# Kernel optimization log

Hardware: AMD Instinct MI355X
Metric: run time of the kernel (lower is better)

The kernel has to match this reference:

```python
import jax, jax.numpy as jnp
import numpy as np

EPS = 1e-5

def _conv1x1(x, w):
    # x: (B, Cin, N, K), w: (Cout, Cin) -> (B, Cout, N, K)
    return jnp.einsum('oc,bcnk->bonk', w, x)

def _bn2d(x, gamma, beta):
    # eval-mode BN with running_mean=0, running_var=1 (fresh init)
    scale = gamma / jnp.sqrt(1.0 + EPS)
    return x * scale[None, :, None, None] + beta[None, :, None, None]

def setup_inputs() -> dict:
    key = jax.random.key(0)
    ks = jax.random.split(key, 10)
    B, Cin, N, K = 8, 64, 1024, 32
    Cout, M = 64, 8
    Cin2 = 2 * Cin  # kernel_input='w_neighbor'
    features = jax.random.normal(ks[0], (B, Cin, N, K), dtype=jnp.float32)
    points_xyz = jax.random.normal(ks[1], (B, 3, N, K), dtype=jnp.float32)
    # ScoreNet convs: mlp_channels [7,16,16,16,M]; first 3 have BN (no bias), last has bias
    w1 = jax.random.normal(ks[2], (16, 7), dtype=jnp.float32) * (2.0 / 7) ** 0.5
    w2 = jax.random.normal(ks[3], (16, 16), dtype=jnp.float32) * (2.0 / 16) ** 0.5
    w3 = jax.random.normal(ks[4], (16, 16), dtype=jnp.float32) * (2.0 / 16) ** 0.5
    w4 = jax.random.normal(ks[5], (M, 16), dtype=jnp.float32) * (2.0 / 16) ** 0.5
    b4 = jnp.zeros((M,), dtype=jnp.float32)
    g1 = jnp.ones((16,), jnp.float32); be1 = jnp.zeros((16,), jnp.float32)
    g2 = jnp.ones((16,), jnp.float32); be2 = jnp.zeros((16,), jnp.float32)
    g3 = jnp.ones((16,), jnp.float32); be3 = jnp.zeros((16,), jnp.float32)
    # weight bank: kaiming_normal on (M, 2Cin, Cout) -> stored as (2Cin, M, Cout)
    wb = jax.random.normal(ks[6], (Cin2, M, Cout), dtype=jnp.float32) * (2.0 / Cin2) ** 0.5
    bn_g = jnp.ones((Cout,), jnp.float32); bn_b = jnp.zeros((Cout,), jnp.float32)
    return dict(features=features, points_xyz=points_xyz,
                w1=w1, g1=g1, be1=be1, w2=w2, g2=g2, be2=be2,
                w3=w3, g3=g3, be3=be3, w4=w4, b4=b4,
                weight_bank=wb, bn_g=bn_g, bn_b=bn_b)

def reference(features, points_xyz, w1, g1, be1, w2, g2, be2, w3, g3, be3,
              w4, b4, weight_bank, bn_g, bn_b):
    B, Cin, N, K = features.shape
    M = weight_bank.shape[1]
    # kernel_input = 'w_neighbor': concat(feat - center, feat) -> (B, 2Cin, N, K)
    center_f = features[..., :1]
    feat = jnp.concatenate([features - center_f, features], axis=1)
    # scorenet input = 'w_neighbor_dist': (center_xyz, xyz_diff, dist) -> (B, 7, N, K)
    center_xyz = jnp.broadcast_to(points_xyz[..., :1], points_xyz.shape)
    xyz_diff = points_xyz - center_xyz
    dist = jnp.sqrt(jnp.sum(xyz_diff * xyz_diff, axis=1, keepdims=True))
    xyz_feats = jnp.concatenate([center_xyz, xyz_diff, dist], axis=1)
    h = jax.nn.relu(_bn2d(_conv1x1(xyz_feats, w1), g1, be1))
    h = jax.nn.relu(_bn2d(_conv1x1(h, w2), g2, be2))
    h = jax.nn.relu(_bn2d(_conv1x1(h, w3), g3, be3))
    s = _conv1x1(h, w4) + b4[None, :, None, None]  # (B, M, N, K)
    scores = jax.nn.softmax(s, axis=1)
    scores = jnp.transpose(scores, (0, 2, 3, 1))  # (B, N, K, M)
    # matmul with weight bank then score-weighted sum over kernels, fused via einsum
    # original: (B,N,K,2Cin)@(2Cin,M*Cout) -> (B,N,K,M,Cout); sum_m scores * . -> (B,N,K,Cout)
    new_features = jnp.einsum('bcnk,cmo,bnkm->bonk', feat, weight_bank, scores)
    # BN2d (eval, fresh stats) + ReLU
    new_features = jax.nn.relu(_bn2d(new_features, bn_g, bn_b))
    return new_features
```

## Files before the change

kernel.cpp:

```cpp
#include <hip/hip_runtime.h>
#include <hip/hip_bf16.h>

typedef _Float16 f16;
typedef __attribute__((ext_vector_type(2))) _Float16 f16x2;
typedef __attribute__((ext_vector_type(8))) _Float16 f16x8;
typedef __attribute__((ext_vector_type(16))) float f32x16;

#define BNSCL 0.9999950000375f

__global__ __launch_bounds__(512) void k_pre(
    const float* __restrict__ xyz,
    const float* __restrict__ w1, const float* __restrict__ g1, const float* __restrict__ be1,
    const float* __restrict__ w2, const float* __restrict__ g2, const float* __restrict__ be2,
    const float* __restrict__ w3, const float* __restrict__ g3, const float* __restrict__ be3,
    const float* __restrict__ w4, const float* __restrict__ b4,
    const float* __restrict__ wb, f16* __restrict__ wbtA,
    const float* __restrict__ feat, f16* __restrict__ Gt,
    f16* __restrict__ scores)
{
    __shared__ __align__(16) f16 ldsD[16384];
    __shared__ __align__(16) f16 gscr[8][512];

    const int tid = threadIdx.x;
    const int bx  = blockIdx.x;

    if (bx >= 256) {
        const int gb   = bx - 256;
        const int ot   = gb >> 9;
        const int lane = tid & 63;
        const int wave = tid >> 6;
        const int l31  = lane & 31;
        const int lh   = lane >> 5;

#pragma unroll
        for (int it = 0; it < 4; ++it) {
            int oct = it * 512 + tid;
            int ln  = oct & 63;
            int ks  = oct >> 6;
            int c   = ks * 2 + (ln >> 5);
            int o   = ot * 32 + (ln & 31);
            f16x8 v;
#pragma unroll
            for (int j = 0; j < 8; ++j) v[j] = (f16)wb[(c * 8 + j) * 64 + o];
            *(f16x8*)&ldsD[oct << 3] = v;
        }
        __syncthreads();

        const int window = (gb & 511) * 8 + wave;
        const int ptglob = window * 64;
        const int b      = ptglob >> 15;
        const int ptb    = ptglob & 32767;
        const float* fb  = feat + (size_t)b * 2097152;

        const bool mon  = (l31 < 16);
        const int  mpos = l31 & 7;
        const f16x2 mk0 = { (f16)((mon && mpos == 0) ? 1.f : 0.f),
                            (f16)((mon && mpos == 1) ? 1.f : 0.f) };
        const f16x2 mk1 = { (f16)((mon && mpos == 2) ? 1.f : 0.f),
                            (f16)((mon && mpos == 3) ? 1.f : 0.f) };
        const f16x2 mk2 = { (f16)((mon && mpos == 4) ? 1.f : 0.f),
                            (f16)((mon && mpos == 5) ? 1.f : 0.f) };
        const f16x2 mk3 = { (f16)((mon && mpos == 6) ? 1.f : 0.f),
                            (f16)((mon && mpos == 7) ? 1.f : 0.f) };

        f32x16 accG = {};
        const f16* Ad = ldsD + (lane << 3);

#pragma unroll
        for (int kk = 0; kk < 32; ++kk) {
            f16x8 aD = *(const f16x8*)(Ad + ((size_t)kk << 9));
            const float* frow = fb + ((size_t)(2 * kk + lh) << 15) + ptb;
            float fcs = (l31 & 8) ? frow[32] : frow[0];
            f16 hC = (f16)(-fcs);
            f16x2 fg2 = {hC, hC};
            f16x2 q0 = mk0 * fg2, q1 = mk1 * fg2, q2 = mk2 * fg2, q3 = mk3 * fg2;
            f16x8 bG = {q0[0],q0[1],q1[0],q1[1],q2[0],q2[1],q3[0],q3[1]};
            accG = __builtin_amdgcn_mfma_f32_32x32x16_f16(aD, bG, accG, 0, 0, 0);
        }

        if (l31 < 16) {
            const int base = (l31 >> 3) * 256 + (l31 & 7);
#pragma unroll
            for (int r = 0; r < 16; ++r) {
                int o = (r & 3) + ((r >> 2) << 3) + (lh << 2);
                gscr[wave][base + o * 8] = (f16)accG[r];
            }
        }
        asm volatile("s_waitcnt lgkmcnt(0)" ::: "memory");
        __builtin_amdgcn_sched_barrier(0);
        {
            f16x8 gv = *(const f16x8*)&gscr[wave][lh * 256 + l31 * 8];
            size_t gg = (size_t)(window * 2 + lh);
            *(f16x8*)&Gt[(gg * 64 + ot * 32 + l31) * 8] = gv;
        }
        return;
    }

    if (bx < 128) {
        int idx = bx * 512 + tid;
        int j    = idx & 7;
        int lane = (idx >> 3) & 63;
        int ks   = (idx >> 9) & 31;
        int bank = (idx >> 14) & 1;
        int ot   = idx >> 15;
        int c    = ks * 2 + (lane >> 5);
        int o    = ot * 32 + (lane & 31);
        float vD = wb[(c * 8 + j) * 64 + o];
        float v  = bank ? vD : vD + wb[((c + 64) * 8 + j) * 64 + o];
        wbtA[idx] = (f16)v;
    }

    float in7[2][7], h1[2][16], h2[2][16], s[2][8];

#pragma unroll
    for (int q = 0; q < 2; ++q) {
        int g = bx * 1024 + q * 512 + tid;
        int b = g >> 15;
        int p = g & 32767;
        int pc = p & ~31;
        const float* xb = xyz + (size_t)b * 98304;
        float cx = xb[pc], cy = xb[32768 + pc], cz = xb[65536 + pc];
        float dx = xb[p] - cx, dy = xb[32768 + p] - cy, dz = xb[65536 + p] - cz;
        in7[q][0] = cx; in7[q][1] = cy; in7[q][2] = cz;
        in7[q][3] = dx; in7[q][4] = dy; in7[q][5] = dz;
        in7[q][6] = sqrtf(dx * dx + dy * dy + dz * dz);
    }

#pragma unroll
    for (int o = 0; o < 16; ++o) {
        float a0 = 0.f, a1 = 0.f;
#pragma unroll
        for (int c = 0; c < 7; ++c) {
            float w = w1[o * 7 + c];
            a0 += w * in7[0][c]; a1 += w * in7[1][c];
        }
        float gs = g1[o] * BNSCL, bb = be1[o];
        h1[0][o] = fmaxf(a0 * gs + bb, 0.f);
        h1[1][o] = fmaxf(a1 * gs + bb, 0.f);
    }
#pragma unroll
    for (int o = 0; o < 16; ++o) {
        float a0 = 0.f, a1 = 0.f;
#pragma unroll
        for (int c = 0; c < 16; ++c) {
            float w = w2[o * 16 + c];
            a0 += w * h1[0][c]; a1 += w * h1[1][c];
        }
        float gs = g2[o] * BNSCL, bb = be2[o];
        h2[0][o] = fmaxf(a0 * gs + bb, 0.f);
        h2[1][o] = fmaxf(a1 * gs + bb, 0.f);
    }
#pragma unroll
    for (int o = 0; o < 16; ++o) {
        float a0 = 0.f, a1 = 0.f;
#pragma unroll
        for (int c = 0; c < 16; ++c) {
            float w = w3[o * 16 + c];
            a0 += w * h2[0][c]; a1 += w * h2[1][c];
        }
        float gs = g3[o] * BNSCL, bb = be3[o];
        h1[0][o] = fmaxf(a0 * gs + bb, 0.f);
        h1[1][o] = fmaxf(a1 * gs + bb, 0.f);
    }
#pragma unroll
    for (int o = 0; o < 8; ++o) {
        float bb = b4[o];
        float a0 = bb, a1 = bb;
#pragma unroll
        for (int c = 0; c < 16; ++c) {
            float w = w4[o * 16 + c];
            a0 += w * h1[0][c]; a1 += w * h1[1][c];
        }
        s[0][o] = a0; s[1][o] = a1;
    }

#pragma unroll
    for (int q = 0; q < 2; ++q) {
        int g = bx * 1024 + q * 512 + tid;
        float mx = s[q][0];
#pragma unroll
        for (int i = 1; i < 8; ++i) mx = fmaxf(mx, s[q][i]);
        float sum = 0.f;
#pragma unroll
        for (int i = 0; i < 8; ++i) { s[q][i] = __expf(s[q][i] - mx); sum += s[q][i]; }
        float inv = 1.f / sum;
        f16x8 o8;
#pragma unroll
        for (int i = 0; i < 8; ++i) o8[i] = (f16)(s[q][i] * inv);
        *(f16x8*)(scores + (size_t)g * 8) = o8;
    }
}

__global__ __launch_bounds__(1024, 4) void k_main(
    const float* __restrict__ feat,
    const f16* __restrict__ scores,
    const f16* __restrict__ wbtA,
    const f16* __restrict__ Gt,
    const float* __restrict__ bn_g, const float* __restrict__ bn_b,
    float* __restrict__ out)
{
    __shared__ __align__(16) f16 lwb[16384];
    __shared__ __align__(16) float fbuf[8][2][1024];

    const int tid  = threadIdx.x;
    const int lane = tid & 63;
    const int wave = tid >> 6;
    const int l31  = lane & 31;
    const int lh   = lane >> 5;
    const int w64  = wave * 64;

    const int ot = blockIdx.x >> 8;
    const int g  = blockIdx.x & 255;
    const int pblock = g * 1024;
    const int b    = pblock >> 15;
    const int pt0  = (pblock & 32767) + w64;
    const int pc0  = pt0 + l31;
    const int pc1  = pc0 + 32;

    const float* fb = feat + (size_t)b * 2097152;
    const float* gsrc0 = fb + (pblock & 32767) + w64 + lane;

    const f16* src = wbtA + ot * 32768;
#pragma unroll
    for (int it = 0; it < 2; ++it) {
        int idx = it * 1024 + tid;
        *(int4*)&lwb[idx << 3] = *(const int4*)&src[idx << 3];
    }

    const int gpt = pblock + w64 + l31;
    f16x8 sv0 = *(const f16x8*)(scores + (size_t)gpt * 8);
    f16x8 sv1 = *(const f16x8*)(scores + (size_t)(gpt + 32) * 8);
    const f16x2 s0a = {sv0[0], sv0[1]}, s0b = {sv0[2], sv0[3]},
                s0c = {sv0[4], sv0[5]}, s0d = {sv0[6], sv0[7]};
    const f16x2 s1a = {sv1[0], sv1[1]}, s1b = {sv1[2], sv1[3]},
                s1c = {sv1[4], sv1[5]}, s1d = {sv1[6], sv1[7]};

    f32x16 acc0 = {}, acc1 = {};
    const f16* Alds = lwb + (lane << 3);

#define STAGE(t)                                                               \
    {                                                                          \
        __builtin_amdgcn_global_load_lds(                                      \
            (const __attribute__((address_space(1))) void*)                    \
                (gsrc0 + ((size_t)(2 * (t)) << 15)),                           \
            (__attribute__((address_space(3))) void*)&fbuf[(t) & 7][0][w64],   \
            4, 0, 0);                                                          \
        __builtin_amdgcn_global_load_lds(                                      \
            (const __attribute__((address_space(1))) void*)                    \
                (gsrc0 + ((size_t)(2 * (t) + 1) << 15)),                       \
            (__attribute__((address_space(3))) void*)&fbuf[(t) & 7][1][w64],   \
            4, 0, 0);                                                          \
    }

#define WAITV(n) asm volatile("s_waitcnt vmcnt(" #n ")" ::: "memory")

    __builtin_amdgcn_sched_barrier(0);
    STAGE(0); STAGE(1); STAGE(2); STAGE(3); STAGE(4); STAGE(5);

    asm volatile("s_waitcnt lgkmcnt(0)" ::: "memory");
    __builtin_amdgcn_s_barrier();

#define KSTEP(kk)                                                              \
    {                                                                          \
        f16x8 aS = *(const f16x8*)(Alds + ((size_t)(kk) << 9));                \
        const float* frow = fbuf[(kk) & 7][lh];                                \
        float fv0 = frow[w64 + l31], fv1 = frow[w64 + l31 + 32];               \
        f16 hR0 = (f16)fv0, hR1 = (f16)fv1;                                    \
        f16x2 fR0 = {hR0, hR0}, fR1 = {hR1, hR1};                              \
        f16x2 r0a = fR0 * s0a, r0b = fR0 * s0b, r0c = fR0 * s0c, r0d = fR0 * s0d; \
        f16x2 r1a = fR1 * s1a, r1b = fR1 * s1b, r1c = fR1 * s1c, r1d = fR1 * s1d; \
        f16x8 bS0 = {r0a[0],r0a[1],r0b[0],r0b[1],r0c[0],r0c[1],r0d[0],r0d[1]}; \
        f16x8 bS1 = {r1a[0],r1a[1],r1b[0],r1b[1],r1c[0],r1c[1],r1d[0],r1d[1]}; \
        acc0 = __builtin_amdgcn_mfma_f32_32x32x16_f16(aS, bS0, acc0, 0, 0, 0); \
        acc1 = __builtin_amdgcn_mfma_f32_32x32x16_f16(aS, bS1, acc1, 0, 0, 0); \
    }

#define PAIR(p)                                                                \
    STAGE(2 * (p) + 6) STAGE(2 * (p) + 7)                                      \
    WAITV(12);                                                                 \
    KSTEP(2 * (p)) KSTEP(2 * (p) + 1)

    PAIR(0)  PAIR(1)  PAIR(2)  PAIR(3)
    PAIR(4)  PAIR(5)  PAIR(6)  PAIR(7)
    PAIR(8)  PAIR(9)  PAIR(10) PAIR(11)
    PAIR(12)
    WAITV(8);
    KSTEP(26) KSTEP(27)
    WAITV(4);
    KSTEP(28) KSTEP(29)
    WAITV(0);
    KSTEP(30) KSTEP(31)
#undef PAIR
#undef KSTEP
#undef STAGE
#undef WAITV

    __builtin_amdgcn_sched_barrier(0);

    {
        const int g0 = (pblock + w64) >> 5;
        const f16x8 a2 = *(const f16x8*)
            &Gt[((size_t)(g0 + lh) * 64 + ot * 32 + l31) * 8];
        f16x8 z8 = {};
        f16x8 bC0 = lh ? z8 : sv0;
        f16x8 bC1 = lh ? sv1 : z8;
        acc0 = __builtin_amdgcn_mfma_f32_32x32x16_f16(a2, bC0, acc0, 0, 0, 0);
        acc1 = __builtin_amdgcn_mfma_f32_32x32x16_f16(a2, bC1, acc1, 0, 0, 0);
    }

#pragma unroll
    for (int r = 0; r < 16; ++r) {
        int o = ot * 32 + (r & 3) + ((r >> 2) << 3) + (lh << 2);
        float gs = bn_g[o] * BNSCL, bb = bn_b[o];
        size_t row = (size_t)(b * 64 + o) << 15;
        out[row + pc0] = fmaxf(acc0[r] * gs + bb, 0.f);
        out[row + pc1] = fmaxf(acc1[r] * gs + bb, 0.f);
    }
}

extern "C" void kernel_launch(void* const* d_in, const int* in_sizes, int n_in,
                              void* d_out, int out_size, void* d_ws, size_t ws_size,
                              hipStream_t stream)
{
    const float* features = (const float*)d_in[0];
    const float* xyz      = (const float*)d_in[1];
    const float* w1  = (const float*)d_in[2];
    const float* g1  = (const float*)d_in[3];
    const float* be1 = (const float*)d_in[4];
    const float* w2  = (const float*)d_in[5];
    const float* g2  = (const float*)d_in[6];
    const float* be2 = (const float*)d_in[7];
    const float* w3  = (const float*)d_in[8];
    const float* g3  = (const float*)d_in[9];
    const float* be3 = (const float*)d_in[10];
    const float* w4  = (const float*)d_in[11];
    const float* b4  = (const float*)d_in[12];
    const float* wb  = (const float*)d_in[13];
    const float* bn_g = (const float*)d_in[14];
    const float* bn_b = (const float*)d_in[15];

    f16* scores = (f16*)d_ws;
    f16* wbtA   = (f16*)((char*)d_ws + (4u << 20));
    f16* Gt     = (f16*)((char*)d_ws + (4u << 20) + 131072);

    k_pre<<<1280, 512, 0, stream>>>(xyz, w1, g1, be1, w2, g2, be2,
                                    w3, g3, be3, w4, b4, wb, wbtA,
                                    features, Gt, scores);
    k_main<<<512, 1024, 0, stream>>>(features, scores, wbtA, Gt,
                                     bn_g, bn_b, (float*)d_out);
}
```

Measured before the change: 188.6 us.

## Compute both output-channel halves per block and loop windows in G precompute

k_main now has each block cover all 64 output channels, with two accumulator sets per wave against both weight-bank halves held in LDS. This halves the grid and means each feature tile is streamed from global memory once instead of twice. k_pre's G blocks each loop over 8 windows per wave, which cuts that grid from 1024 to 128 blocks and amortizes the weight transpose into LDS. The cost is double the LDS and accumulator registers in k_main, lower occupancy, and only 256 blocks, which may leave CUs underused.

```diff
diff --git a/kernel.cpp b/kernel.cpp
--- a/kernel.cpp
+++ b/kernel.cpp
@@ -26,7 +26,7 @@
 
     if (bx >= 256) {
         const int gb   = bx - 256;
-        const int ot   = gb >> 9;
+        const int ot   = gb >> 6;
         const int lane = tid & 63;
         const int wave = tid >> 6;
         const int l31  = lane & 31;
@@ -45,12 +45,6 @@
             *(f16x8*)&ldsD[oct << 3] = v;
         }
         __syncthreads();
-
-        const int window = (gb & 511) * 8 + wave;
-        const int ptglob = window * 64;
-        const int b      = ptglob >> 15;
-        const int ptb    = ptglob & 32767;
-        const float* fb  = feat + (size_t)b * 2097152;
 
         const bool mon  = (l31 < 16);
         const int  mpos = l31 & 7;
@@ -63,35 +57,46 @@
         const f16x2 mk3 = { (f16)((mon && mpos == 6) ? 1.f : 0.f),
                             (f16)((mon && mpos == 7) ? 1.f : 0.f) };
 
-        f32x16 accG = {};
         const f16* Ad = ldsD + (lane << 3);
 
-#pragma unroll
-        for (int kk = 0; kk < 32; ++kk) {
-            f16x8 aD = *(const f16x8*)(Ad + ((size_t)kk << 9));
-            const float* frow = fb + ((size_t)(2 * kk + lh) << 15) + ptb;
-            float fcs = (l31 & 8) ? frow[32] : frow[0];
-            f16 hC = (f16)(-fcs);
-            f16x2 fg2 = {hC, hC};
-            f16x2 q0 = mk0 * fg2, q1 = mk1 * fg2, q2 = mk2 * fg2, q3 = mk3 * fg2;
-            f16x8 bG = {q0[0],q0[1],q1[0],q1[1],q2[0],q2[1],q3[0],q3[1]};
-            accG = __builtin_amdgcn_mfma_f32_32x32x16_f16(aD, bG, accG, 0, 0, 0);
-        }
-
-        if (l31 < 16) {
-            const int base = (l31 >> 3) * 256 + (l31 & 7);
-#pragma unroll
-            for (int r = 0; r < 16; ++r) {
-                int o = (r & 3) + ((r >> 2) << 3) + (lh << 2);
-                gscr[wave][base + o * 8] = (f16)accG[r];
+#pragma unroll 1
+        for (int w = 0; w < 8; ++w) {
+            const int window = (gb & 63) * 64 + wave * 8 + w;
+            const int ptglob = window * 64;
+            const int b      = ptglob >> 15;
+            const int ptb    = ptglob & 32767;
+            const float* fb  = feat + (size_t)b * 2097152;
+
+            f32x16 accG = {};
+#pragma unroll
+            for (int kk = 0; kk < 32; ++kk) {
+                f16x8 aD = *(const f16x8*)(Ad + ((size_t)kk << 9));
+                const float* frow = fb + ((size_t)(2 * kk + lh) << 15) + ptb;
+                float fcs = (l31 & 8) ? frow[32] : frow[0];
+                f16 hC = (f16)(-fcs);
+                f16x2 fg2 = {hC, hC};
+                f16x2 q0 = mk0 * fg2, q1 = mk1 * fg2,
+                      q2 = mk2 * fg2, q3 = mk3 * fg2;
+                f16x8 bG = {q0[0],q0[1],q1[0],q1[1],q2[0],q2[1],q3[0],q3[1]};
+                accG = __builtin_amdgcn_mfma_f32_32x32x16_f16(aD, bG, accG, 0, 0, 0);
             }
-        }
-        asm volatile("s_waitcnt lgkmcnt(0)" ::: "memory");
-        __builtin_amdgcn_sched_barrier(0);
-        {
-            f16x8 gv = *(const f16x8*)&gscr[wave][lh * 256 + l31 * 8];
-            size_t gg = (size_t)(window * 2 + lh);
-            *(f16x8*)&Gt[(gg * 64 + ot * 32 + l31) * 8] = gv;
+
+            if (l31 < 16) {
+                const int base = (l31 >> 3) * 256 + (l31 & 7);
+#pragma unroll
+                for (int r = 0; r < 16; ++r) {
+                    int o = (r & 3) + ((r >> 2) << 3) + (lh << 2);
+                    gscr[wave][base + o * 8] = (f16)accG[r];
+                }
+            }
+            asm volatile("s_waitcnt lgkmcnt(0)" ::: "memory");
+            __builtin_amdgcn_sched_barrier(0);
+            {
+                f16x8 gv = *(const f16x8*)&gscr[wave][lh * 256 + l31 * 8];
+                size_t gg = (size_t)(window * 2 + lh);
+                *(f16x8*)&Gt[(gg * 64 + ot * 32 + l31) * 8] = gv;
+            }
+            asm volatile("s_waitcnt lgkmcnt(0)" ::: "memory");
         }
         return;
     }
@@ -199,7 +204,7 @@
     const float* __restrict__ bn_g, const float* __restrict__ bn_b,
     float* __restrict__ out)
 {
-    __shared__ __align__(16) f16 lwb[16384];
+    __shared__ __align__(16) f16 lwb[32768];
     __shared__ __align__(16) float fbuf[8][2][1024];
 
     const int tid  = threadIdx.x;
@@ -209,8 +214,7 @@
     const int lh   = lane >> 5;
     const int w64  = wave * 64;
 
-    const int ot = blockIdx.x >> 8;
-    const int g  = blockIdx.x & 255;
+    const int g  = blockIdx.x;
     const int pblock = g * 1024;
     const int b    = pblock >> 15;
     const int pt0  = (pblock & 32767) + w64;
@@ -220,11 +224,11 @@
     const float* fb = feat + (size_t)b * 2097152;
     const float* gsrc0 = fb + (pblock & 32767) + w64 + lane;
 
-    const f16* src = wbtA + ot * 32768;
 #pragma unroll
     for (int it = 0; it < 2; ++it) {
         int idx = it * 1024 + tid;
-        *(int4*)&lwb[idx << 3] = *(const int4*)&src[idx << 3];
+        *(int4*)&lwb[idx << 3] = *(const int4*)&wbtA[idx << 3];
+        *(int4*)&lwb[16384 + (idx << 3)] = *(const int4*)&wbtA[32768 + (idx << 3)];
     }
 
     const int gpt = pblock + w64 + l31;
@@ -235,7 +239,8 @@
     const f16x2 s1a = {sv1[0], sv1[1]}, s1b = {sv1[2], sv1[3]},
                 s1c = {sv1[4], sv1[5]}, s1d = {sv1[6], sv1[7]};
 
-    f32x16 acc0 = {}, acc1 = {};
+    f32x16 accA0 = {}, accA1 = {};
+    f32x16 accB0 = {}, accB1 = {};
     const f16* Alds = lwb + (lane << 3);
 
 #define STAGE(t)                                                               \
@@ -262,7 +267,8 @@
 
 #define KSTEP(kk)                                                              \
     {                                                                          \
-        f16x8 aS = *(const f16x8*)(Alds + ((size_t)(kk) << 9));                \
+        f16x8 aS0 = *(const f16x8*)(Alds + ((size_t)(kk) << 9));               \
+        f16x8 aS1 = *(const f16x8*)(Alds + 16384 + ((size_t)(kk) << 9));       \
         const float* frow = fbuf[(kk) & 7][lh];                                \
         float fv0 = frow[w64 + l31], fv1 = frow[w64 + l31 + 32];               \
         f16 hR0 = (f16)fv0, hR1 = (f16)fv1;                                    \
@@ -271,8 +277,10 @@
         f16x2 r1a = fR1 * s1a, r1b = fR1 * s1b, r1c = fR1 * s1c, r1d = fR1 * s1d; \
         f16x8 bS0 = {r0a[0],r0a[1],r0b[0],r0b[1],r0c[0],r0c[1],r0d[0],r0d[1]}; \
         f16x8 bS1 = {r1a[0],r1a[1],r1b[0],r1b[1],r1c[0],r1c[1],r1d[0],r1d[1]}; \
-        acc0 = __builtin_amdgcn_mfma_f32_32x32x16_f16(aS, bS0, acc0, 0, 0, 0); \
-        acc1 = __builtin_amdgcn_mfma_f32_32x32x16_f16(aS, bS1, acc1, 0, 0, 0); \
+        accA0 = __builtin_amdgcn_mfma_f32_32x32x16_f16(aS0, bS0, accA0, 0, 0, 0); \
+        accA1 = __builtin_amdgcn_mfma_f32_32x32x16_f16(aS0, bS1, accA1, 0, 0, 0); \
+        accB0 = __builtin_amdgcn_mfma_f32_32x32x16_f16(aS1, bS0, accB0, 0, 0, 0); \
+        accB1 = __builtin_amdgcn_mfma_f32_32x32x16_f16(aS1, bS1, accB1, 0, 0, 0); \
     }
 
 #define PAIR(p)                                                                \
@@ -299,22 +307,34 @@
 
     {
         const int g0 = (pblock + w64) >> 5;
-        const f16x8 a2 = *(const f16x8*)
-            &Gt[((size_t)(g0 + lh) * 64 + ot * 32 + l31) * 8];
+        const f16* gtb = Gt + ((size_t)(g0 + lh) * 64 + l31) * 8;
+        const f16x8 a2_0 = *(const f16x8*)gtb;
+        const f16x8 a2_1 = *(const f16x8*)(gtb + 256);
         f16x8 z8 = {};
         f16x8 bC0 = lh ? z8 : sv0;
         f16x8 bC1 = lh ? sv1 : z8;
-        acc0 = __builtin_amdgcn_mfma_f32_32x32x16_f16(a2, bC0, acc0, 0, 0, 0);
-        acc1 = __builtin_amdgcn_mfma_f32_32x32x16_f16(a2, bC1, acc1, 0, 0, 0);
+        accA0 = __builtin_amdgcn_mfma_f32_32x32x16_f16(a2_0, bC0, accA0, 0, 0, 0);
+        accA1 = __builtin_amdgcn_mfma_f32_32x32x16_f16(a2_0, bC1, accA1, 0, 0, 0);
+        accB0 = __builtin_amdgcn_mfma_f32_32x32x16_f16(a2_1, bC0, accB0, 0, 0, 0);
+        accB1 = __builtin_amdgcn_mfma_f32_32x32x16_f16(a2_1, bC1, accB1, 0, 0, 0);
     }
 
 #pragma unroll
     for (int r = 0; r < 16; ++r) {
-        int o = ot * 32 + (r & 3) + ((r >> 2) << 3) + (lh << 2);
-        float gs = bn_g[o] * BNSCL, bb = bn_b[o];
-        size_t row = (size_t)(b * 64 + o) << 15;
-        out[row + pc0] = fmaxf(acc0[r] * gs + bb, 0.f);
-        out[row + pc1] = fmaxf(acc1[r] * gs + bb, 0.f);
+        int oo = (r & 3) + ((r >> 2) << 3) + (lh << 2);
+        {
+            float gs = bn_g[oo] * BNSCL, bb = bn_b[oo];
+            size_t row = (size_t)(b * 64 + oo) << 15;
+            out[row + pc0] = fmaxf(accA0[r] * gs + bb, 0.f);
+            out[row + pc1] = fmaxf(accA1[r] * gs + bb, 0.f);
+        }
+        {
+            int o1 = 32 + oo;
+            float gs = bn_g[o1] * BNSCL, bb = bn_b[o1];
+            size_t row = (size_t)(b * 64 + o1) << 15;
+            out[row + pc0] = fmaxf(accB0[r] * gs + bb, 0.f);
+            out[row + pc1] = fmaxf(accB1[r] * gs + bb, 0.f);
+        }
     }
 }
 
@@ -343,9 +363,9 @@
     f16* wbtA   = (f16*)((char*)d_ws + (4u << 20));
     f16* Gt     = (f16*)((char*)d_ws + (4u << 20) + 131072);
 
-    k_pre<<<1280, 512, 0, stream>>>(xyz, w1, g1, be1, w2, g2, be2,
-                                    w3, g3, be3, w4, b4, wb, wbtA,
-                                    features, Gt, scores);
-    k_main<<<512, 1024, 0, stream>>>(features, scores, wbtA, Gt,
+    k_pre<<<384, 512, 0, stream>>>(xyz, w1, g1, be1, w2, g2, be2,
+                                   w3, g3, be3, w4, b4, wb, wbtA,
+                                   features, Gt, scores);
+    k_main<<<256, 1024, 0, stream>>>(features, scores, wbtA, Gt,
                                      bn_g, bn_b, (float*)d_out);
 }
```

Result: no change. 188.4 us (-0.1%).
